# Optimization experiments

Hardware: AMD Instinct MI355X
Metric: run time of the kernel (lower is better)

Reference implementation:

```python
import jax, jax.numpy as jnp
import numpy as np

KERNEL = (3, 3)
STRIDE = (1, 1)


def setup_inputs() -> dict:
    key = jax.random.key(0)
    k1, k2 = jax.random.split(key)
    x = jax.random.normal(k1, (8, 32, 32, 64), dtype=jnp.float32)
    # unshared weights: [H_out, W_out, C_in*kh*kw, C_out]
    lc_params = jax.random.normal(k2, (30, 30, 64 * 3 * 3, 64), dtype=jnp.float32) * 0.02
    return {"x": x, "lc_params": lc_params}


def reference(x, lc_params):
    # im2col patch extraction; feature dim ordered [C_in, kh, kw] (C slowest),
    # exactly matching the layout the original param tensor is trained against.
    x_unf = jax.lax.conv_general_dilated_patches(
        lhs=x,
        filter_shape=KERNEL,
        window_strides=STRIDE,
        padding='VALID',
        dimension_numbers=('NHWC', 'HWIO', 'NHWC'),
    )  # [B, H_out, W_out, C*kh*kw]
    # per-location contraction; same math as (x_unf[..., None] * lc_params).sum(3)
    # but lowered as a batched matmul instead of materializing [B,H,W,K,O].
    out = jnp.einsum('bhwk,hwko->bhwo', x_unf, lc_params)
    return out
```

## Files before the change

kernel.cpp:

```cpp
#include <hip/hip_runtime.h>


#define HO 30
#define WO 30
#define HI 32
#define WI 32
#define CI 64
#define CO 64
#define BATCH 8
#define KTOT 576

__global__ __launch_bounds__(256) void lc_kernel(const float* __restrict__ x,
                                                 const float* __restrict__ wgt,
                                                 float* __restrict__ out) {
    const int hw = blockIdx.x;
    const int h  = hw / WO;
    const int w  = hw - h * WO;
    const int tid = threadIdx.x;

    __shared__ float smem[8192];
    float* xs = smem;

    #pragma unroll
    for (int it = 0; it < 18; ++it) {
        int idx = it * 256 + tid;
        int c  = idx & 63;
        int t  = idx >> 6;
        int b  = t / 9;
        int r  = t - b * 9;
        int kh = r / 3;
        int kw = r - kh * 3;
        float v = x[((b * HI + h + kh) * WI + (w + kw)) * CI + c];
        xs[b * KTOT + c * 9 + kh * 3 + kw] = v;
    }
    __syncthreads();

    const int o4 = tid & 15;
    const int kg = tid >> 4;

    const float4* w4 = reinterpret_cast<const float4*>(
                           wgt + (size_t)hw * KTOT * CO) + o4;

    float4 acc[BATCH];
    #pragma unroll
    for (int b = 0; b < BATCH; ++b) acc[b] = make_float4(0.f, 0.f, 0.f, 0.f);

    const int k0base = kg * 36;
    for (int i = 0; i < 9; ++i) {
        const int k0 = k0base + 4 * i;
        float4 w0 = w4[(k0 + 0) * 16];
        float4 w1 = w4[(k0 + 1) * 16];
        float4 w2 = w4[(k0 + 2) * 16];
        float4 w3 = w4[(k0 + 3) * 16];
        #pragma unroll
        for (int b = 0; b < BATCH; ++b) {
            float4 xv = *reinterpret_cast<const float4*>(&xs[b * KTOT + k0]);
            acc[b].x = fmaf(xv.x, w0.x, acc[b].x);
            acc[b].y = fmaf(xv.x, w0.y, acc[b].y);
            acc[b].z = fmaf(xv.x, w0.z, acc[b].z);
            acc[b].w = fmaf(xv.x, w0.w, acc[b].w);
            acc[b].x = fmaf(xv.y, w1.x, acc[b].x);
            acc[b].y = fmaf(xv.y, w1.y, acc[b].y);
            acc[b].z = fmaf(xv.y, w1.z, acc[b].z);
            acc[b].w = fmaf(xv.y, w1.w, acc[b].w);
            acc[b].x = fmaf(xv.z, w2.x, acc[b].x);
            acc[b].y = fmaf(xv.z, w2.y, acc[b].y);
            acc[b].z = fmaf(xv.z, w2.z, acc[b].z);
            acc[b].w = fmaf(xv.z, w2.w, acc[b].w);
            acc[b].x = fmaf(xv.w, w3.x, acc[b].x);
            acc[b].y = fmaf(xv.w, w3.y, acc[b].y);
            acc[b].z = fmaf(xv.w, w3.z, acc[b].z);
            acc[b].w = fmaf(xv.w, w3.w, acc[b].w);
        }
    }

    __syncthreads();
    float4* p4 = reinterpret_cast<float4*>(smem);
    #pragma unroll
    for (int b = 0; b < BATCH; ++b) p4[(kg * BATCH + b) * 16 + o4] = acc[b];
    __syncthreads();

    if (tid < 128) {
        int b   = tid >> 4;
        int oo4 = tid & 15;
        float4 s = make_float4(0.f, 0.f, 0.f, 0.f);
        #pragma unroll
        for (int kgi = 0; kgi < 16; ++kgi) {
            float4 v = p4[(kgi * BATCH + b) * 16 + oo4];
            s.x += v.x; s.y += v.y; s.z += v.z; s.w += v.w;
        }
        float* dst = out + (((size_t)b * HO + h) * WO + w) * CO + oo4 * 4;
        *reinterpret_cast<float4*>(dst) = s;
    }
}

extern "C" void kernel_launch(void* const* d_in, const int* in_sizes, int n_in,
                              void* d_out, int out_size, void* d_ws, size_t ws_size,
                              hipStream_t stream) {
    const float* x   = (const float*)d_in[0];
    const float* wgt = (const float*)d_in[1];
    float* out       = (float*)d_out;
    lc_kernel<<<dim3(HO * WO), dim3(256), 0, stream>>>(x, wgt, out);
}
```

Before: 194.5 us.

## Read input directly with wave-uniform loads, split K across waves per channel block

Drops the shared-memory im2col staging of the input patch. Each wave now owns a 16-channel slice of C_in, and each lane owns one output channel. Input values are read straight from global memory at wave-uniform addresses, which can become scalar loads. Weights are loaded as scalar floats coalesced across lanes rather than as float4, and a smaller 4-way cross-wave reduction replaces the 16-way one. The trade-off is less per-thread ILP, no float4 weight loads, and input reads that depend on the compiler turning uniform accesses into scalar loads.

```diff
diff --git a/kernel.cpp b/kernel.cpp
--- a/kernel.cpp
+++ b/kernel.cpp
@@ -16,81 +16,49 @@
     const int hw = blockIdx.x;
     const int h  = hw / WO;
     const int w  = hw - h * WO;
-    const int tid = threadIdx.x;
+    const int tid  = threadIdx.x;
+    const int lane = tid & 63;
+    const int wv   = __builtin_amdgcn_readfirstlane(tid >> 6);
+    const int c0   = wv * 16;
 
-    __shared__ float smem[8192];
-    float* xs = smem;
+    __shared__ float red[4 * BATCH * CO];
 
+    float acc[BATCH];
     #pragma unroll
-    for (int it = 0; it < 18; ++it) {
-        int idx = it * 256 + tid;
-        int c  = idx & 63;
-        int t  = idx >> 6;
-        int b  = t / 9;
-        int r  = t - b * 9;
-        int kh = r / 3;
-        int kw = r - kh * 3;
-        float v = x[((b * HI + h + kh) * WI + (w + kw)) * CI + c];
-        xs[b * KTOT + c * 9 + kh * 3 + kw] = v;
-    }
-    __syncthreads();
+    for (int b = 0; b < BATCH; ++b) acc[b] = 0.f;
 
-    const int o4 = tid & 15;
-    const int kg = tid >> 4;
+    const float* wbase = wgt + (size_t)hw * (KTOT * CO) + lane;
 
-    const float4* w4 = reinterpret_cast<const float4*>(
-                           wgt + (size_t)hw * KTOT * CO) + o4;
+    for (int p = 0; p < 9; ++p) {
+        const int kh = p / 3;
+        const int kw = p - kh * 3;
 
-    float4 acc[BATCH];
-    #pragma unroll
-    for (int b = 0; b < BATCH; ++b) acc[b] = make_float4(0.f, 0.f, 0.f, 0.f);
+        float wreg[16];
+        #pragma unroll
+        for (int cc = 0; cc < 16; ++cc)
+            wreg[cc] = wbase[(size_t)(((c0 + cc) * 9 + p)) * CO];
 
-    const int k0base = kg * 36;
-    for (int i = 0; i < 9; ++i) {
-        const int k0 = k0base + 4 * i;
-        float4 w0 = w4[(k0 + 0) * 16];
-        float4 w1 = w4[(k0 + 1) * 16];
-        float4 w2 = w4[(k0 + 2) * 16];
-        float4 w3 = w4[(k0 + 3) * 16];
         #pragma unroll
         for (int b = 0; b < BATCH; ++b) {
-            float4 xv = *reinterpret_cast<const float4*>(&xs[b * KTOT + k0]);
-            acc[b].x = fmaf(xv.x, w0.x, acc[b].x);
-            acc[b].y = fmaf(xv.x, w0.y, acc[b].y);
-            acc[b].z = fmaf(xv.x, w0.z, acc[b].z);
-            acc[b].w = fmaf(xv.x, w0.w, acc[b].w);
-            acc[b].x = fmaf(xv.y, w1.x, acc[b].x);
-            acc[b].y = fmaf(xv.y, w1.y, acc[b].y);
-            acc[b].z = fmaf(xv.y, w1.z, acc[b].z);
-            acc[b].w = fmaf(xv.y, w1.w, acc[b].w);
-            acc[b].x = fmaf(xv.z, w2.x, acc[b].x);
-            acc[b].y = fmaf(xv.z, w2.y, acc[b].y);
-            acc[b].z = fmaf(xv.z, w2.z, acc[b].z);
-            acc[b].w = fmaf(xv.z, w2.w, acc[b].w);
-            acc[b].x = fmaf(xv.w, w3.x, acc[b].x);
-            acc[b].y = fmaf(xv.w, w3.y, acc[b].y);
-            acc[b].z = fmaf(xv.w, w3.z, acc[b].z);
-            acc[b].w = fmaf(xv.w, w3.w, acc[b].w);
+            const float* xb = x + (((b * HI + h + kh) * WI) + (w + kw)) * CI + c0;
+            #pragma unroll
+            for (int cc = 0; cc < 16; ++cc)
+                acc[b] = fmaf(xb[cc], wreg[cc], acc[b]);
         }
     }
 
-    __syncthreads();
-    float4* p4 = reinterpret_cast<float4*>(smem);
     #pragma unroll
-    for (int b = 0; b < BATCH; ++b) p4[(kg * BATCH + b) * 16 + o4] = acc[b];
+    for (int b = 0; b < BATCH; ++b)
+        red[(wv * BATCH + b) * CO + lane] = acc[b];
     __syncthreads();
 
-    if (tid < 128) {
-        int b   = tid >> 4;
-        int oo4 = tid & 15;
-        float4 s = make_float4(0.f, 0.f, 0.f, 0.f);
-        #pragma unroll
-        for (int kgi = 0; kgi < 16; ++kgi) {
-            float4 v = p4[(kgi * BATCH + b) * 16 + oo4];
-            s.x += v.x; s.y += v.y; s.z += v.z; s.w += v.w;
-        }
-        float* dst = out + (((size_t)b * HO + h) * WO + w) * CO + oo4 * 4;
-        *reinterpret_cast<float4*>(dst) = s;
+    #pragma unroll
+    for (int rep = 0; rep < 2; ++rep) {
+        const int pidx = rep * 256 + tid;
+        const int b = pidx >> 6;
+        const int o = pidx & 63;
+        float s = red[pidx] + red[512 + pidx] + red[1024 + pidx] + red[1536 + pidx];
+        out[(((size_t)b * HO + h) * WO + w) * CO + o] = s;
     }
 }
 
```

New measurement: 198.3 us. Within noise of the previous version (+1.9%).
